# Kernel optimization log

Measured on AMD Instinct MI355X. Metric: run time of the kernel, lower is better.

## Reference

```python
import jax, jax.numpy as jnp
import numpy as np

EPS = 1e-5
NEG_SLOPE = 0.2


def _batched_dynamic_conv(x, kernels):
    # x: [B, C, H, W]; kernels: [B, Cout, Cin, 3, 3]. Per-sample distinct
    # kernels == one grouped conv with feature_group_count = B.
    B, C, H, W = x.shape
    Cout = kernels.shape[1]
    xg = x.reshape(1, B * C, H, W)
    kg = kernels.reshape(B * Cout, C, 3, 3)
    y = jax.lax.conv_general_dilated(
        xg, kg, window_strides=(1, 1), padding=((1, 1), (1, 1)),
        feature_group_count=B,
        dimension_numbers=('NCHW', 'OIHW', 'NCHW'))
    return y.reshape(B, Cout, H, W)


def _instance_norm(y):
    # InstanceNorm2d(affine=False): per (b, c) over spatial dims, biased var.
    mean = jnp.mean(y, axis=(2, 3), keepdims=True)
    var = jnp.var(y, axis=(2, 3), keepdims=True)
    return (y - mean) * jax.lax.rsqrt(var + EPS)


def _leaky_relu(y):
    return jnp.where(y >= 0, y, NEG_SLOPE * y)


def setup_inputs() -> dict:
    key = jax.random.key(0)
    k1, k2, k3 = jax.random.split(key, 3)
    B, C, H, W = 16, 64, 128, 128
    x = jax.random.normal(k1, (B, C, H, W), dtype=jnp.float32)
    kernel1 = jax.random.normal(k2, (B, C, C, 3, 3), dtype=jnp.float32) * 0.05
    kernel2 = jax.random.normal(k3, (B, C, C, 3, 3), dtype=jnp.float32) * 0.05
    return {"x": x, "kernel1": kernel1, "kernel2": kernel2}


def reference(x, kernel1, kernel2):
    h = _leaky_relu(_instance_norm(_batched_dynamic_conv(x, kernel1)))
    h = _instance_norm(_batched_dynamic_conv(h, kernel2))
    return _leaky_relu(x + h)
```

## Files before the change

### kernel.cpp

```cpp
#include <hip/hip_runtime.h>
#include <stdint.h>
#include <stddef.h>

#define BATCH 16
#define CH    64
#define IH    128
#define IW    128
#define HW    (IH*IW)

#define PROW 8320
#define PB   1081600
#define SEG  2112

typedef __attribute__((ext_vector_type(8))) short short8;
typedef __attribute__((ext_vector_type(4))) short short4v;
typedef __attribute__((ext_vector_type(4))) float f32x4;
typedef __attribute__((ext_vector_type(2))) float f32x2;

__device__ __forceinline__ float bf2f(short s) {
    union { unsigned int u; float f; } v;
    v.u = ((unsigned int)(unsigned short)s) << 16;
    return v.f;
}
__device__ __forceinline__ short f2bf(float f) {
    union { float f; unsigned int u; } v; v.f = f;
    unsigned int r = v.u + 0x7fffu + ((v.u >> 16) & 1u);
    return (short)(r >> 16);
}

__device__ __forceinline__ void gload_lds16(const short* g, short* l) {
    __builtin_amdgcn_global_load_lds(
        (const __attribute__((address_space(1))) void*)g,
        (__attribute__((address_space(3))) void*)l, 16, 0, 0);
}

__global__ __launch_bounds__(256) void prep_all(const float* __restrict__ x,
                                                const float* __restrict__ w1,
                                                const float* __restrict__ w2,
                                                short* __restrict__ xpad,
                                                short* __restrict__ w1t,
                                                short* __restrict__ w2t) {
    const int bid = blockIdx.x;
    const int t = threadIdx.x;
    if (bid < 2048) {
        __shared__ float tile[CH * 129];
        const int b = bid >> 7;
        const int y = bid & 127;
        const float* src = x + (size_t)b * CH * HW + (size_t)y * IW;
        #pragma unroll
        for (int i = 0; i < 32; ++i) {
            int lin = i * 256 + t;
            int c = lin >> 7, xx = lin & 127;
            tile[c * 129 + xx] = src[(size_t)c * HW + xx];
        }
        __syncthreads();
        unsigned int* dst = (unsigned int*)(xpad) + (size_t)b * (PB / 2) + (size_t)(y + 1) * (PROW / 2);
        #pragma unroll
        for (int j = 0; j < 16; ++j) {
            int lin = j * 256 + t;
            int c2 = lin & 31, xx = lin >> 5;
            unsigned int lo = (unsigned int)(unsigned short)f2bf(tile[(2 * c2) * 129 + xx]);
            unsigned int hi = (unsigned int)(unsigned short)f2bf(tile[(2 * c2 + 1) * 129 + xx]);
            dst[(c2 >> 4) * 2080 + (xx + 1) * 16 + (c2 & 15)] = lo | (hi << 16);
        }
    } else if (bid < 2560) {
        int b2 = bid - 2048;
        const float* src = w1; short* dst = w1t;
        if (b2 >= 256) { src = w2; dst = w2t; b2 -= 256; }
        int gt = b2 * 256 + t;
        int ci   = gt & 31;
        int cout = (gt >> 5) & 63;
        int cc   = (gt >> 11) & 1;
        int b    = gt >> 12;
        const float* s = src + ((size_t)(b * 64 + cout)) * 576 + (cc * 32 + ci) * 9;
        short* d = dst + ((size_t)(b * 2 + cc) * 9) * 2048 + cout * 32 + ci;
        #pragma unroll
        for (int tap = 0; tap < 9; ++tap)
            d[tap * 2048] = f2bf(s[tap]);
    } else {
        int b2 = bid - 2560;
        short* p = xpad + (size_t)b2 * PB;
        const short8 z = {0,0,0,0,0,0,0,0};
        #pragma unroll
        for (int i = 0; i < 17; ++i) {
            int s = i * 256 + t;
            if (s >= 4128) break;
            if (s < 2080) {
                int row = (s < 1040) ? 0 : 129;
                int o = (s < 1040 ? s : s - 1040) * 8;
                *(short8*)&p[(size_t)row * PROW + o] = z;
            } else {
                int u = s - 2080;
                int k = u & 3, col = (u >> 2) & 1, cc = (u >> 3) & 1, pr = (u >> 4) + 1;
                *(short8*)&p[(size_t)pr * PROW + cc * 4160 + (col ? 129 * 32 : 0) + k * 8] = z;
            }
        }
    }
}

template<bool FUSED>
__global__ __launch_bounds__(256, 3) void conv_kernel(
    const short* __restrict__ in, const short* __restrict__ wt,
    short* __restrict__ out, const float* __restrict__ nrm,
    float* __restrict__ part_s, float* __restrict__ part_q) {

    __shared__ short act[12 * SEG];

    const int b    = blockIdx.y;
    const int t    = threadIdx.x;
    const int lane = t & 63;
    const int wave = t >> 6;
    const int l15  = lane & 15;
    const int q    = lane >> 4;
    const int bx   = blockIdx.x >> 1;
    const int ph2  = blockIdx.x & 1;
    const int xp0  = ph2 * 64;
    const int y0   = bx * 4 + wave;

    const short* inB = in + (size_t)b * PB;
    const short* wgl = wt + (size_t)b * 36864;
    const int aoff = l15 * 32 + q * 8;

    short8 a2[2][4];
    #pragma unroll
    for (int mi = 0; mi < 4; ++mi)
        a2[0][mi] = *(const short8*)&wgl[aoff + mi * 512];

    if (!FUSED) {
        #pragma unroll
        for (int k = 0; k < 3; ++k) {
            const int s = wave + k * 4;
            const int rg = bx * 4 + (s >> 1);
            const short* gseg = inB + (size_t)rg * PROW + (s & 1) * 4160 + xp0 * 32;
            short* lseg = &act[s * SEG];
            #pragma unroll
            for (int c = 0; c < 4; ++c)
                gload_lds16(gseg + c * 512 + lane * 8, lseg + c * 512);
            if (lane < 8)
                gload_lds16(gseg + 2048 + lane * 8, lseg + 2048);
        }
    } else {
        const int scc = wave & 1;
        const int ci0 = (lane & 3) * 8;
        f32x2 sb[8];
        #pragma unroll
        for (int j = 0; j < 8; ++j)
            sb[j] = ((const f32x2*)nrm)[b * CH + scc * 32 + ci0 + j];
        #pragma unroll
        for (int k = 0; k < 3; ++k) {
            const int s = wave + k * 4;
            const int rg = bx * 4 + (s >> 1);
            const bool rowpad = (rg == 0) || (rg == 129);
            const short* gseg = inB + (size_t)rg * PROW + scc * 4160 + xp0 * 32;
            short* lseg = &act[s * SEG];
            #pragma unroll
            for (int c = 0; c < 5; ++c) {
                if (c < 4 || lane < 8) {
                    short8 v = *(const short8*)&gseg[c * 512 + lane * 8];
                    const int lpx = c * 16 + (lane >> 2);
                    const bool xm = (ph2 == 0 && lpx == 0) || (ph2 == 1 && lpx == 65);
                    short8 o;
                    if (rowpad || xm) {
                        o = (short8){0,0,0,0,0,0,0,0};
                    } else {
                        #pragma unroll
                        for (int j = 0; j < 8; ++j) {
                            float f = sb[j].x * bf2f(v[j]) + sb[j].y;
                            f = f >= 0.f ? f : 0.2f * f;
                            o[j] = f2bf(f);
                        }
                    }
                    *(short8*)&lseg[c * 512 + lane * 8] = o;
                }
            }
        }
    }
    __syncthreads();

    const f32x4 zero4 = {0.f, 0.f, 0.f, 0.f};
    f32x4 acc[4][4];
    #pragma unroll
    for (int mi = 0; mi < 4; ++mi)
        #pragma unroll
        for (int ni = 0; ni < 4; ++ni) acc[mi][ni] = zero4;

    #pragma unroll
    for (int s = 0; s < 18; ++s) {
        const int cc = s / 9, tap = s % 9;
        const int dy = tap / 3, dx = tap % 3;
        if (s + 1 < 18) {
            const short* anext = wgl + (s + 1) * 2048 + aoff;
            #pragma unroll
            for (int mi = 0; mi < 4; ++mi)
                a2[(s + 1) & 1][mi] = *(const short8*)&anext[mi * 512];
        }
        const int segb = ((wave + dy) * 2 + cc) * SEG;
        short8 bb[4];
        #pragma unroll
        for (int ni = 0; ni < 4; ++ni)
            bb[ni] = *(const short8*)&act[segb + (dx + ni * 16 + l15) * 32 + q * 8];
        #pragma unroll
        for (int mi = 0; mi < 4; ++mi)
            #pragma unroll
            for (int ni = 0; ni < 4; ++ni)
                acc[mi][ni] = __builtin_amdgcn_mfma_f32_16x16x32_bf16(
                    a2[s & 1][mi], bb[ni], acc[mi][ni], 0, 0, 0);
    }

    const int pbase = ((b * 128 + y0) * 2 + ph2) * 64;
    #pragma unroll
    for (int mi = 0; mi < 4; ++mi) {
        float psum[4] = {0.f,0.f,0.f,0.f};
        float psq[4]  = {0.f,0.f,0.f,0.f};
        #pragma unroll
        for (int ni = 0; ni < 4; ++ni) {
            int xx = xp0 + ni * 16 + l15;
            size_t base = (size_t)b * PB + (size_t)(1 + y0) * PROW
                          + (mi >> 1) * 4160 + (size_t)(1 + xx) * 32
                          + (mi & 1) * 16 + q * 4;
            short4v o;
            #pragma unroll
            for (int g = 0; g < 4; ++g) {
                float v = acc[mi][ni][g];
                o[g] = f2bf(v);
                psum[g] += v;
                psq[g]  += v * v;
            }
            *(short4v*)&out[base] = o;
        }
        #pragma unroll
        for (int g = 0; g < 4; ++g) {
            float s = psum[g], s2 = psq[g];
            #pragma unroll
            for (int off = 1; off < 16; off <<= 1) {
                s  += __shfl_xor(s,  off, 64);
                s2 += __shfl_xor(s2, off, 64);
            }
            if (l15 == 0) {
                int idx = pbase + mi * 16 + q * 4 + g;
                part_s[idx] = s;
                part_q[idx] = s2;
            }
        }
    }
}

__global__ __launch_bounds__(256) void finalize_stats(const float* __restrict__ part_s,
                                                      const float* __restrict__ part_q,
                                                      float* __restrict__ nrm) {
    __shared__ float red[2][4][64];
    const int b = blockIdx.x;
    const int c = threadIdx.x & 63;
    const int g = threadIdx.x >> 6;
    const float* ps = part_s + (size_t)b * 16384 + c;
    const float* pq = part_q + (size_t)b * 16384 + c;
    float s = 0.f, s2 = 0.f;
    #pragma unroll 8
    for (int r = 0; r < 64; ++r) {
        s  += ps[(g * 64 + r) * 64];
        s2 += pq[(g * 64 + r) * 64];
    }
    red[0][g][c] = s;
    red[1][g][c] = s2;
    __syncthreads();
    if (threadIdx.x < 64) {
        float S = red[0][0][c] + red[0][1][c] + red[0][2][c] + red[0][3][c];
        float Q = red[1][0][c] + red[1][1][c] + red[1][2][c] + red[1][3][c];
        const float inv = 1.0f / (float)HW;
        float mean = S * inv;
        float var = Q * inv - mean * mean;
        float scale = rsqrtf(var + 1e-5f);
        f32x2 sb = {scale, -mean * scale};
        ((f32x2*)nrm)[b * CH + c] = sb;
    }
}

__global__ __launch_bounds__(256) void final_kernel(const float* __restrict__ x,
                                                    const short* __restrict__ y2,
                                                    const float* __restrict__ nrm,
                                                    float* __restrict__ out) {
    __shared__ float tile[64 * 65];
    const int x0 = blockIdx.x * 64;
    const int y  = blockIdx.y;
    const int b  = blockIdx.z;
    const int t  = threadIdx.x;
    const f32x2* nb = (const f32x2*)nrm + b * CH;
    const size_t rowb = (size_t)b * PB + (size_t)(y + 1) * PROW;
    #pragma unroll
    for (int i = 0; i < 2; ++i) {
        int s = i * 256 + t;
        int xx = s >> 3;
        int c0 = (s & 7) * 8;
        int cc = c0 >> 5, cl = c0 & 31;
        short8 v = *(const short8*)&y2[rowb + cc * 4160 + (size_t)(x0 + xx + 1) * 32 + cl];
        #pragma unroll
        for (int j = 0; j < 8; ++j) {
            f32x2 sb = nb[c0 + j];
            tile[(c0 + j) * 65 + xx] = sb.x * bf2f(v[j]) + sb.y;
        }
    }
    __syncthreads();
    #pragma unroll
    for (int i = 0; i < 4; ++i) {
        int lin = i * 1024 + t * 4;
        int c = lin >> 6;
        int xx = lin & 63;
        size_t g = ((size_t)(b * CH + c) * IH + y) * IW + x0 + xx;
        f32x4 xv = *(const f32x4*)&x[g];
        f32x4 o;
        #pragma unroll
        for (int k = 0; k < 4; ++k) {
            float f = xv[k] + tile[c * 65 + xx + k];
            o[k] = f >= 0.f ? f : 0.2f * f;
        }
        *(f32x4*)&out[g] = o;
    }
}

extern "C" void kernel_launch(void* const* d_in, const int* in_sizes, int n_in,
                              void* d_out, int out_size, void* d_ws, size_t ws_size,
                              hipStream_t stream) {
    const float* x  = (const float*)d_in[0];
    const float* w1 = (const float*)d_in[1];
    const float* w2 = (const float*)d_in[2];
    float* out = (float*)d_out;
    char* ws = (char*)d_ws;

    const size_t SZ_PAD  = 34611200ull;
    const size_t SZ_PART = 1048576ull;
    short* xpad = (short*)(ws);
    short* hpad = (short*)(ws + SZ_PAD);
    short* w1t  = (short*)(ws + 2 * SZ_PAD);
    short* w2t  = (short*)(ws + 2 * SZ_PAD + 1179648ull);
    float* ps1  = (float*)(ws + 2 * SZ_PAD + 2359296ull);
    float* pq1  = (float*)(ws + 2 * SZ_PAD + 2359296ull + SZ_PART);
    float* ps2  = (float*)(ws + 2 * SZ_PAD + 2359296ull + 2 * SZ_PART);
    float* pq2  = (float*)(ws + 2 * SZ_PAD + 2359296ull + 3 * SZ_PART);
    float* nrm1 = (float*)(ws + 2 * SZ_PAD + 2359296ull + 4 * SZ_PART);
    float* nrm2 = nrm1 + BATCH * CH * 2;

    if (ws_size < 2 * SZ_PAD + 2359296ull + 4 * SZ_PART + 8192) return;

    prep_all<<<2576, 256, 0, stream>>>(x, w1, w2, xpad, w1t, w2t);
    conv_kernel<false><<<dim3(64, 16), 256, 0, stream>>>(xpad, w1t, hpad, nullptr, ps1, pq1);
    finalize_stats<<<16, 256, 0, stream>>>(ps1, pq1, nrm1);
    conv_kernel<true><<<dim3(64, 16), 256, 0, stream>>>(hpad, w2t, xpad, nrm1, ps2, pq2);
    finalize_stats<<<16, 256, 0, stream>>>(ps2, pq2, nrm2);
    final_kernel<<<dim3(2, 128, 16), 256, 0, stream>>>(x, xpad, nrm2, out);
}
```

Before: 231.0 us.

## Make conv kernel persistent over four tiles with double-buffered LDS prefetch

The conv kernel now launches 256 blocks, one per CU-sized chunk, and each block loops over four tiles. Each tile's input is prefetched into a second LDS buffer while the current tile's MFMA loop runs; the fused variant stages loads in registers and writes the normalized activations after compute. Occupancy drops to one block per CU, trading latency hiding from multiple resident blocks for explicit software pipelining. It also adds register pressure from the 15-entry staging array.

```diff
diff --git a/kernel.cpp b/kernel.cpp
--- a/kernel.cpp
+++ b/kernel.cpp
@@ -99,64 +99,85 @@
 }
 
 template<bool FUSED>
-__global__ __launch_bounds__(256, 3) void conv_kernel(
+__global__ __launch_bounds__(256, 1) void conv_kernel(
     const short* __restrict__ in, const short* __restrict__ wt,
     short* __restrict__ out, const float* __restrict__ nrm,
     float* __restrict__ part_s, float* __restrict__ part_q) {
 
-    __shared__ short act[12 * SEG];
-
-    const int b    = blockIdx.y;
+    __shared__ short act[2][12 * SEG];
+
+    const int g    = blockIdx.x;
+    const int b    = g >> 4;
     const int t    = threadIdx.x;
     const int lane = t & 63;
     const int wave = t >> 6;
     const int l15  = lane & 15;
     const int q    = lane >> 4;
-    const int bx   = blockIdx.x >> 1;
-    const int ph2  = blockIdx.x & 1;
-    const int xp0  = ph2 * 64;
-    const int y0   = bx * 4 + wave;
 
     const short* inB = in + (size_t)b * PB;
     const short* wgl = wt + (size_t)b * 36864;
     const int aoff = l15 * 32 + q * 8;
 
-    short8 a2[2][4];
-    #pragma unroll
-    for (int mi = 0; mi < 4; ++mi)
-        a2[0][mi] = *(const short8*)&wgl[aoff + mi * 512];
-
-    if (!FUSED) {
+    const int scc = wave & 1;
+    f32x2 sb[8];
+    if (FUSED) {
+        const int ci0 = (lane & 3) * 8;
+        #pragma unroll
+        for (int j = 0; j < 8; ++j)
+            sb[j] = ((const f32x2*)nrm)[b * CH + scc * 32 + ci0 + j];
+    }
+
+    short8 stg[15];
+
+
+    auto stage_issue = [&](int tt, short* buf) {
+        const int xp0 = (tt & 1) * 64;
+        const int quad = ((g & 15) << 1) + (tt >> 1);
         #pragma unroll
         for (int k = 0; k < 3; ++k) {
             const int s = wave + k * 4;
-            const int rg = bx * 4 + (s >> 1);
+            const int rg = quad * 4 + (s >> 1);
             const short* gseg = inB + (size_t)rg * PROW + (s & 1) * 4160 + xp0 * 32;
-            short* lseg = &act[s * SEG];
+            short* lseg = buf + s * SEG;
             #pragma unroll
             for (int c = 0; c < 4; ++c)
                 gload_lds16(gseg + c * 512 + lane * 8, lseg + c * 512);
             if (lane < 8)
                 gload_lds16(gseg + 2048 + lane * 8, lseg + 2048);
         }
-    } else {
-        const int scc = wave & 1;
-        const int ci0 = (lane & 3) * 8;
-        f32x2 sb[8];
-        #pragma unroll
-        for (int j = 0; j < 8; ++j)
-            sb[j] = ((const f32x2*)nrm)[b * CH + scc * 32 + ci0 + j];
+    };
+
+    auto stage_load = [&](int tt) {
+        const int xp0 = (tt & 1) * 64;
+        const int quad = ((g & 15) << 1) + (tt >> 1);
         #pragma unroll
         for (int k = 0; k < 3; ++k) {
             const int s = wave + k * 4;
-            const int rg = bx * 4 + (s >> 1);
+            const int rg = quad * 4 + (s >> 1);
+            const short* gseg = inB + (size_t)rg * PROW + (s & 1) * 4160 + xp0 * 32;
+            #pragma unroll
+            for (int c = 0; c < 5; ++c) {
+                short8 v = {0,0,0,0,0,0,0,0};
+                if (c < 4 || lane < 8)
+                    v = *(const short8*)&gseg[c * 512 + lane * 8];
+                stg[k * 5 + c] = v;
+            }
+        }
+    };
+
+    auto stage_write = [&](int tt, short* buf) {
+        const int ph2 = tt & 1;
+        const int quad = ((g & 15) << 1) + (tt >> 1);
+        #pragma unroll
+        for (int k = 0; k < 3; ++k) {
+            const int s = wave + k * 4;
+            const int rg = quad * 4 + (s >> 1);
             const bool rowpad = (rg == 0) || (rg == 129);
-            const short* gseg = inB + (size_t)rg * PROW + scc * 4160 + xp0 * 32;
-            short* lseg = &act[s * SEG];
+            short* lseg = buf + s * SEG;
             #pragma unroll
             for (int c = 0; c < 5; ++c) {
                 if (c < 4 || lane < 8) {
-                    short8 v = *(const short8*)&gseg[c * 512 + lane * 8];
+                    short8 v = stg[k * 5 + c];
                     const int lpx = c * 16 + (lane >> 2);
                     const bool xm = (ph2 == 0 && lpx == 0) || (ph2 == 1 && lpx == 65);
                     short8 o;
@@ -174,74 +195,100 @@
                 }
             }
         }
-    }
-    __syncthreads();
-
-    const f32x4 zero4 = {0.f, 0.f, 0.f, 0.f};
-    f32x4 acc[4][4];
+    };
+
+    short8 a2[2][4];
     #pragma unroll
     for (int mi = 0; mi < 4; ++mi)
-        #pragma unroll
-        for (int ni = 0; ni < 4; ++ni) acc[mi][ni] = zero4;
-
-    #pragma unroll
-    for (int s = 0; s < 18; ++s) {
-        const int cc = s / 9, tap = s % 9;
-        const int dy = tap / 3, dx = tap % 3;
-        if (s + 1 < 18) {
-            const short* anext = wgl + (s + 1) * 2048 + aoff;
+        a2[0][mi] = *(const short8*)&wgl[aoff + mi * 512];
+
+    if (FUSED) { stage_load(0); stage_write(0, act[0]); }
+    else       stage_issue(0, act[0]);
+    __syncthreads();
+
+    #pragma unroll 1
+    for (int tt = 0; tt < 4; ++tt) {
+        short* bufr = act[tt & 1];
+        short* bufw = act[(tt + 1) & 1];
+
+        if (tt < 3) {
+            if (FUSED) stage_load(tt + 1);
+            else       stage_issue(tt + 1, bufw);
+        }
+
+        const int ph2 = tt & 1;
+        const int quad = ((g & 15) << 1) + (tt >> 1);
+        const int xp0 = ph2 * 64;
+        const int y0 = quad * 4 + wave;
+
+        const f32x4 zero4 = {0.f, 0.f, 0.f, 0.f};
+        f32x4 acc[4][4];
+        #pragma unroll
+        for (int mi = 0; mi < 4; ++mi)
+            #pragma unroll
+            for (int ni = 0; ni < 4; ++ni) acc[mi][ni] = zero4;
+
+        #pragma unroll
+        for (int s = 0; s < 18; ++s) {
+            const int cc = s / 9, tap = s % 9;
+            const int dy = tap / 3, dx = tap % 3;
+            const short* anext = wgl + (((s + 1) % 18) * 2048) + aoff;
             #pragma unroll
             for (int mi = 0; mi < 4; ++mi)
                 a2[(s + 1) & 1][mi] = *(const short8*)&anext[mi * 512];
-        }
-        const int segb = ((wave + dy) * 2 + cc) * SEG;
-        short8 bb[4];
-        #pragma unroll
-        for (int ni = 0; ni < 4; ++ni)
-            bb[ni] = *(const short8*)&act[segb + (dx + ni * 16 + l15) * 32 + q * 8];
-        #pragma unroll
-        for (int mi = 0; mi < 4; ++mi)
+            const int segb = ((wave + dy) * 2 + cc) * SEG;
+            short8 bb[4];
             #pragma unroll
             for (int ni = 0; ni < 4; ++ni)
-                acc[mi][ni] = __builtin_amdgcn_mfma_f32_16x16x32_bf16(
-                    a2[s & 1][mi], bb[ni], acc[mi][ni], 0, 0, 0);
-    }
-
-    const int pbase = ((b * 128 + y0) * 2 + ph2) * 64;
-    #pragma unroll
-    for (int mi = 0; mi < 4; ++mi) {
-        float psum[4] = {0.f,0.f,0.f,0.f};
-        float psq[4]  = {0.f,0.f,0.f,0.f};
-        #pragma unroll
-        for (int ni = 0; ni < 4; ++ni) {
-            int xx = xp0 + ni * 16 + l15;
-            size_t base = (size_t)b * PB + (size_t)(1 + y0) * PROW
-                          + (mi >> 1) * 4160 + (size_t)(1 + xx) * 32
-                          + (mi & 1) * 16 + q * 4;
-            short4v o;
-            #pragma unroll
-            for (int g = 0; g < 4; ++g) {
-                float v = acc[mi][ni][g];
-                o[g] = f2bf(v);
-                psum[g] += v;
-                psq[g]  += v * v;
-            }
-            *(short4v*)&out[base] = o;
-        }
-        #pragma unroll
-        for (int g = 0; g < 4; ++g) {
-            float s = psum[g], s2 = psq[g];
-            #pragma unroll
-            for (int off = 1; off < 16; off <<= 1) {
-                s  += __shfl_xor(s,  off, 64);
-                s2 += __shfl_xor(s2, off, 64);
-            }
-            if (l15 == 0) {
-                int idx = pbase + mi * 16 + q * 4 + g;
-                part_s[idx] = s;
-                part_q[idx] = s2;
-            }
-        }
+                bb[ni] = *(const short8*)&bufr[segb + (dx + ni * 16 + l15) * 32 + q * 8];
+            #pragma unroll
+            for (int mi = 0; mi < 4; ++mi)
+                #pragma unroll
+                for (int ni = 0; ni < 4; ++ni)
+                    acc[mi][ni] = __builtin_amdgcn_mfma_f32_16x16x32_bf16(
+                        a2[s & 1][mi], bb[ni], acc[mi][ni], 0, 0, 0);
+        }
+
+        if (FUSED && tt < 3) stage_write(tt + 1, bufw);
+
+        const int pbase = ((b * 128 + y0) * 2 + ph2) * 64;
+        #pragma unroll
+        for (int mi = 0; mi < 4; ++mi) {
+            float psum[4] = {0.f,0.f,0.f,0.f};
+            float psq[4]  = {0.f,0.f,0.f,0.f};
+            #pragma unroll
+            for (int ni = 0; ni < 4; ++ni) {
+                int xx = xp0 + ni * 16 + l15;
+                size_t base = (size_t)b * PB + (size_t)(1 + y0) * PROW
+                              + (mi >> 1) * 4160 + (size_t)(1 + xx) * 32
+                              + (mi & 1) * 16 + q * 4;
+                short4v o;
+                #pragma unroll
+                for (int gg = 0; gg < 4; ++gg) {
+                    float v = acc[mi][ni][gg];
+                    o[gg] = f2bf(v);
+                    psum[gg] += v;
+                    psq[gg]  += v * v;
+                }
+                *(short4v*)&out[base] = o;
+            }
+            #pragma unroll
+            for (int gg = 0; gg < 4; ++gg) {
+                float s = psum[gg], s2 = psq[gg];
+                #pragma unroll
+                for (int off = 1; off < 16; off <<= 1) {
+                    s  += __shfl_xor(s,  off, 64);
+                    s2 += __shfl_xor(s2, off, 64);
+                }
+                if (l15 == 0) {
+                    int idx = pbase + mi * 16 + q * 4 + gg;
+                    part_s[idx] = s;
+                    part_q[idx] = s2;
+                }
+            }
+        }
+
+        __syncthreads();
     }
 }
 
@@ -342,9 +389,9 @@
     if (ws_size < 2 * SZ_PAD + 2359296ull + 4 * SZ_PART + 8192) return;
 
     prep_all<<<2576, 256, 0, stream>>>(x, w1, w2, xpad, w1t, w2t);
-    conv_kernel<false><<<dim3(64, 16), 256, 0, stream>>>(xpad, w1t, hpad, nullptr, ps1, pq1);
+    conv_kernel<false><<<256, 256, 0, stream>>>(xpad, w1t, hpad, nullptr, ps1, pq1);
     finalize_stats<<<16, 256, 0, stream>>>(ps1, pq1, nrm1);
-    conv_kernel<true><<<dim3(64, 16), 256, 0, stream>>>(hpad, w2t, xpad, nrm1, ps2, pq2);
+    conv_kernel<true><<<256, 256, 0, stream>>>(hpad, w2t, xpad, nrm1, ps2, pq2);
     finalize_stats<<<16, 256, 0, stream>>>(ps2, pq2, nrm2);
     final_kernel<<<dim3(2, 128, 16), 256, 0, stream>>>(x, xpad, nrm2, out);
 }
```

After: 243.3 us. 5.3% more time.

## Split output channels across waves and halve rows per conv block

Applied to the files above, without the earlier changes.

Each conv block now covers 2 output rows instead of 4. Its four waves split into two row groups, and each wave computes 32 of the 64 output channels instead of all 64. The grid doubles to 128x16 blocks, LDS per block shrinks to 8 segments, launch bounds rise to 4 blocks per CU, and the double-buffered weight prefetch is replaced by direct per-step loads. The aim is more blocks and occupancy with fewer accumulator registers, at the cost of a larger halo re-read fraction (2 extra rows per 2 rows instead of per 4) and weights loaded without prefetch.

```diff
diff --git a/kernel.cpp b/kernel.cpp
--- a/kernel.cpp
+++ b/kernel.cpp
@@ -99,88 +99,80 @@
 }
 
 template<bool FUSED>
-__global__ __launch_bounds__(256, 3) void conv_kernel(
+__global__ __launch_bounds__(256, 4) void conv_kernel(
     const short* __restrict__ in, const short* __restrict__ wt,
     short* __restrict__ out, const float* __restrict__ nrm,
     float* __restrict__ part_s, float* __restrict__ part_q) {
 
-    __shared__ short act[12 * SEG];
+    __shared__ short act[8 * SEG];
 
     const int b    = blockIdx.y;
+    const int bq   = blockIdx.x >> 1;
+    const int ph2  = blockIdx.x & 1;
+    const int xp0  = ph2 * 64;
     const int t    = threadIdx.x;
     const int lane = t & 63;
     const int wave = t >> 6;
     const int l15  = lane & 15;
     const int q    = lane >> 4;
-    const int bx   = blockIdx.x >> 1;
-    const int ph2  = blockIdx.x & 1;
-    const int xp0  = ph2 * 64;
-    const int y0   = bx * 4 + wave;
+    const int ch   = wave & 1;
+    const int wr   = wave >> 1;
+    const int y0   = bq * 2 + wr;
 
     const short* inB = in + (size_t)b * PB;
-    const short* wgl = wt + (size_t)b * 36864;
-    const int aoff = l15 * 32 + q * 8;
-
-    short8 a2[2][4];
-    #pragma unroll
-    for (int mi = 0; mi < 4; ++mi)
-        a2[0][mi] = *(const short8*)&wgl[aoff + mi * 512];
-
-    if (!FUSED) {
-        #pragma unroll
-        for (int k = 0; k < 3; ++k) {
+
+    {
+        #pragma unroll
+        for (int k = 0; k < 2; ++k) {
             const int s = wave + k * 4;
-            const int rg = bx * 4 + (s >> 1);
+            const int rg = bq * 2 + (s >> 1);
             const short* gseg = inB + (size_t)rg * PROW + (s & 1) * 4160 + xp0 * 32;
             short* lseg = &act[s * SEG];
-            #pragma unroll
-            for (int c = 0; c < 4; ++c)
-                gload_lds16(gseg + c * 512 + lane * 8, lseg + c * 512);
-            if (lane < 8)
-                gload_lds16(gseg + 2048 + lane * 8, lseg + 2048);
-        }
-    } else {
-        const int scc = wave & 1;
-        const int ci0 = (lane & 3) * 8;
-        f32x2 sb[8];
-        #pragma unroll
-        for (int j = 0; j < 8; ++j)
-            sb[j] = ((const f32x2*)nrm)[b * CH + scc * 32 + ci0 + j];
-        #pragma unroll
-        for (int k = 0; k < 3; ++k) {
-            const int s = wave + k * 4;
-            const int rg = bx * 4 + (s >> 1);
-            const bool rowpad = (rg == 0) || (rg == 129);
-            const short* gseg = inB + (size_t)rg * PROW + scc * 4160 + xp0 * 32;
-            short* lseg = &act[s * SEG];
-            #pragma unroll
-            for (int c = 0; c < 5; ++c) {
-                if (c < 4 || lane < 8) {
-                    short8 v = *(const short8*)&gseg[c * 512 + lane * 8];
-                    const int lpx = c * 16 + (lane >> 2);
-                    const bool xm = (ph2 == 0 && lpx == 0) || (ph2 == 1 && lpx == 65);
-                    short8 o;
-                    if (rowpad || xm) {
-                        o = (short8){0,0,0,0,0,0,0,0};
-                    } else {
-                        #pragma unroll
-                        for (int j = 0; j < 8; ++j) {
-                            float f = sb[j].x * bf2f(v[j]) + sb[j].y;
-                            f = f >= 0.f ? f : 0.2f * f;
-                            o[j] = f2bf(f);
+            if (!FUSED) {
+                #pragma unroll
+                for (int c = 0; c < 4; ++c)
+                    gload_lds16(gseg + c * 512 + lane * 8, lseg + c * 512);
+                if (lane < 8)
+                    gload_lds16(gseg + 2048 + lane * 8, lseg + 2048);
+            } else {
+                const bool rowpad = (rg == 0) || (rg == 129);
+                const int ci0 = (lane & 3) * 8;
+                f32x2 sb[8];
+                #pragma unroll
+                for (int j = 0; j < 8; ++j)
+                    sb[j] = ((const f32x2*)nrm)[b * CH + (wave & 1) * 32 + ci0 + j];
+                #pragma unroll
+                for (int c = 0; c < 5; ++c) {
+                    if (c < 4 || lane < 8) {
+                        short8 v = *(const short8*)&gseg[c * 512 + lane * 8];
+                        const int lpx = c * 16 + (lane >> 2);
+                        const bool xm = (ph2 == 0 && lpx == 0) || (ph2 == 1 && lpx == 65);
+                        short8 o;
+                        if (rowpad || xm) {
+                            o = (short8){0,0,0,0,0,0,0,0};
+                        } else {
+                            #pragma unroll
+                            for (int j = 0; j < 8; ++j) {
+                                float f = sb[j].x * bf2f(v[j]) + sb[j].y;
+                                f = f >= 0.f ? f : 0.2f * f;
+                                o[j] = f2bf(f);
+                            }
                         }
+                        *(short8*)&lseg[c * 512 + lane * 8] = o;
                     }
-                    *(short8*)&lseg[c * 512 + lane * 8] = o;
                 }
             }
         }
     }
     __syncthreads();
 
+    const short* wgl = wt + (size_t)b * 36864;
+    const int aoff = ch * 1024 + l15 * 32 + q * 8;
+
     const f32x4 zero4 = {0.f, 0.f, 0.f, 0.f};
-    f32x4 acc[4][4];
-    #pragma unroll
-    for (int mi = 0; mi < 4; ++mi)
+    f32x4 acc[2][4];
+    #pragma unroll
+    for (int mi = 0; mi < 2; ++mi)
         #pragma unroll
         for (int ni = 0; ni < 4; ++ni) acc[mi][ni] = zero4;
 
@@ -188,36 +180,34 @@
     for (int s = 0; s < 18; ++s) {
         const int cc = s / 9, tap = s % 9;
         const int dy = tap / 3, dx = tap % 3;
-        if (s + 1 < 18) {
-            const short* anext = wgl + (s + 1) * 2048 + aoff;
-            #pragma unroll
-            for (int mi = 0; mi < 4; ++mi)
-                a2[(s + 1) & 1][mi] = *(const short8*)&anext[mi * 512];
-        }
-        const int segb = ((wave + dy) * 2 + cc) * SEG;
-        short8 bb[4];
+        const short* arow = wgl + s * 2048 + aoff;
+        const int segb = ((wr + dy) * 2 + cc) * SEG;
+        short8 a[2], bb[4];
+        #pragma unroll
+        for (int mi = 0; mi < 2; ++mi)
+            a[mi] = *(const short8*)&arow[mi * 512];
         #pragma unroll
         for (int ni = 0; ni < 4; ++ni)
             bb[ni] = *(const short8*)&act[segb + (dx + ni * 16 + l15) * 32 + q * 8];
         #pragma unroll
-        for (int mi = 0; mi < 4; ++mi)
+        for (int mi = 0; mi < 2; ++mi)
             #pragma unroll
             for (int ni = 0; ni < 4; ++ni)
                 acc[mi][ni] = __builtin_amdgcn_mfma_f32_16x16x32_bf16(
-                    a2[s & 1][mi], bb[ni], acc[mi][ni], 0, 0, 0);
+                    a[mi], bb[ni], acc[mi][ni], 0, 0, 0);
     }
 
     const int pbase = ((b * 128 + y0) * 2 + ph2) * 64;
     #pragma unroll
-    for (int mi = 0; mi < 4; ++mi) {
+    for (int mi = 0; mi < 2; ++mi) {
         float psum[4] = {0.f,0.f,0.f,0.f};
         float psq[4]  = {0.f,0.f,0.f,0.f};
         #pragma unroll
         for (int ni = 0; ni < 4; ++ni) {
             int xx = xp0 + ni * 16 + l15;
             size_t base = (size_t)b * PB + (size_t)(1 + y0) * PROW
-                          + (mi >> 1) * 4160 + (size_t)(1 + xx) * 32
-                          + (mi & 1) * 16 + q * 4;
+                          + ch * 4160 + (size_t)(1 + xx) * 32
+                          + mi * 16 + q * 4;
             short4v o;
             #pragma unroll
             for (int g = 0; g < 4; ++g) {
@@ -237,7 +227,7 @@
                 s2 += __shfl_xor(s2, off, 64);
             }
             if (l15 == 0) {
-                int idx = pbase + mi * 16 + q * 4 + g;
+                int idx = pbase + ch * 32 + mi * 16 + q * 4 + g;
                 part_s[idx] = s;
                 part_q[idx] = s2;
             }
@@ -342,9 +332,9 @@
     if (ws_size < 2 * SZ_PAD + 2359296ull + 4 * SZ_PART + 8192) return;
 
     prep_all<<<2576, 256, 0, stream>>>(x, w1, w2, xpad, w1t, w2t);
-    conv_kernel<false><<<dim3(64, 16), 256, 0, stream>>>(xpad, w1t, hpad, nullptr, ps1, pq1);
+    conv_kernel<false><<<dim3(128, 16), 256, 0, stream>>>(xpad, w1t, hpad, nullptr, ps1, pq1);
     finalize_stats<<<16, 256, 0, stream>>>(ps1, pq1, nrm1);
-    conv_kernel<true><<<dim3(64, 16), 256, 0, stream>>>(hpad, w2t, xpad, nrm1, ps2, pq2);
+    conv_kernel<true><<<dim3(128, 16), 256, 0, stream>>>(hpad, w2t, xpad, nrm1, ps2, pq2);
     finalize_stats<<<16, 256, 0, stream>>>(ps2, pq2, nrm2);
     final_kernel<<<dim3(2, 128, 16), 256, 0, stream>>>(x, xpad, nrm2, out);
 }
```

New measurement: 238.1 us. 3.1% more time.
